# Optimization experiments

Hardware: AMD Instinct MI355X
Metric: run time of the kernel (lower is better)

Reference implementation:

```python
import jax, jax.numpy as jnp
import numpy as np

STRIDES = (8, 16, 32)
IMG = 640
REG_MAX = 16
TOPK = 10
ALPHA = 0.5
BETA = 6.0
EPS_IOU = 1e-16


def _make_anchors():
    # anchor centers for all pyramid levels, (N, 2) in pixel coords
    pts = []
    for s in STRIDES:
        h = w = IMG // s
        ys, xs = jnp.meshgrid(jnp.arange(h, dtype=jnp.float32),
                              jnp.arange(w, dtype=jnp.float32), indexing='ij')
        a = (jnp.stack([xs, ys], axis=-1).reshape(-1, 2) + 0.5) * s
        pts.append(a)
    return jnp.concatenate(pts, axis=0)  # (8400, 2)


def _iou_pairwise(pred, gt):
    # pred (B,N,4), gt (B,M,4) -> IoU (B,M,N)
    b1 = pred[:, None, :, :]   # (B,1,N,4)
    b2 = gt[:, :, None, :]     # (B,M,1,4)
    tl = jnp.maximum(b1[..., :2], b2[..., :2])
    br = jnp.minimum(b1[..., 2:], b2[..., 2:])
    wh = jnp.clip(br - tl, 0.0)
    inter = wh[..., 0] * wh[..., 1]
    a1 = (b1[..., 2] - b1[..., 0]) * (b1[..., 3] - b1[..., 1])
    a2 = (b2[..., 2] - b2[..., 0]) * (b2[..., 3] - b2[..., 1])
    return inter / (a1 + a2 - inter + EPS_IOU)


def _iou_1v1(b1, b2):
    # elementwise IoU, both (..., 4)
    tl = jnp.maximum(b1[..., :2], b2[..., :2])
    br = jnp.minimum(b1[..., 2:], b2[..., 2:])
    wh = jnp.clip(br - tl, 0.0)
    inter = wh[..., 0] * wh[..., 1]
    a1 = (b1[..., 2] - b1[..., 0]) * (b1[..., 3] - b1[..., 1])
    a2 = (b2[..., 2] - b2[..., 0]) * (b2[..., 3] - b2[..., 1])
    return inter / (a1 + a2 - inter + EPS_IOU)


def setup_inputs() -> dict:
    key = jax.random.key(0)
    ks = jax.random.split(key, 6)
    B, N, NC, M = 32, 8400, 80, 40
    pred_scores = jax.random.normal(ks[0], (B, N, NC), jnp.float32)
    pred_dist = jax.random.normal(ks[1], (B, N, 4 * REG_MAX), jnp.float32)
    gt_labels = jax.random.randint(ks[2], (B, M, 1), 0, NC, dtype=jnp.int32)
    cxy = jax.random.uniform(ks[3], (B, M, 2), jnp.float32) * 560.0 + 40.0
    wh = jax.random.uniform(ks[4], (B, M, 2), jnp.float32) * 120.0 + 20.0
    gt_bboxes = jnp.concatenate([jnp.clip(cxy - wh / 2, 0.0, float(IMG)),
                                 jnp.clip(cxy + wh / 2, 0.0, float(IMG))], axis=-1)
    dfl_weight = jax.random.normal(ks[5], (REG_MAX,), jnp.float32) * 0.05
    return {"pred_scores": pred_scores, "pred_dist": pred_dist,
            "gt_labels": gt_labels, "gt_bboxes": gt_bboxes,
            "dfl_weight": dfl_weight}


def reference(pred_scores, pred_dist, gt_labels, gt_bboxes, dfl_weight):
    B, N, NC = pred_scores.shape
    M = gt_bboxes.shape[1]
    anchors = _make_anchors()  # (N, 2)

    # DFL: softmax over reg bins, weighted sum with (random-init) conv weight
    prob = jax.nn.softmax(pred_dist.reshape(B, N, 4, REG_MAX), axis=-1)
    ltrb = prob @ dfl_weight                      # (B,N,4)
    pred_bboxes = jnp.concatenate([anchors - ltrb[..., :2],
                                   anchors + ltrb[..., 2:]], axis=-1)  # (B,N,4) xyxy

    # ---- task-aligned assigner (no-grad) ----
    sg = jax.lax.stop_gradient
    sig = jax.nn.sigmoid(sg(pred_scores))         # (B,N,NC)
    labels = gt_labels[..., 0].astype(jnp.int32)  # (B,M)
    sigT = jnp.swapaxes(sig, 1, 2)                # (B,NC,N)
    scores = jnp.take_along_axis(sigT, jnp.broadcast_to(labels[:, :, None], (B, M, N)), axis=1)  # (B,M,N)
    ious = jnp.clip(_iou_pairwise(sg(pred_bboxes), gt_bboxes), 0.0)      # (B,M,N)
    align = scores ** ALPHA * ious ** BETA        # (B,M,N)

    _, topk_idxs = jax.lax.top_k(align, TOPK)     # (B,M,TOPK) over anchors
    mask = jnp.zeros((B * M, N), dtype=align.dtype)
    mask = mask.at[jnp.arange(B * M)[:, None], topk_idxs.reshape(B * M, TOPK)].set(1.0)
    mask = mask.reshape(B, M, N)
    mask = mask * (align > 1e-9).astype(align.dtype)
    max_m = align.max(axis=1)                     # (B,N) best metric per anchor
    mask = mask * (align == max_m[:, None, :]).astype(align.dtype)

    fg_mask = mask.max(axis=1)                    # (B,N) in {0,1}
    tgt_idx = mask.argmax(axis=1)                 # (B,N) assigned gt index
    ts_sum = jnp.maximum(fg_mask.sum(), 1.0)

    # ---- classification targets (vectorized scatter) ----
    asg_labels = jnp.take_along_axis(labels, tgt_idx, axis=1)  # (B,N)
    target_scores = jax.nn.one_hot(asg_labels, NC, dtype=pred_scores.dtype) * (max_m * fg_mask)[..., None]

    x = pred_scores
    bce = jnp.maximum(x, 0.0) - x * target_scores + jnp.log1p(jnp.exp(-jnp.abs(x)))
    loss_cls = bce.sum() / ts_sum

    # ---- box IoU loss on positives (vectorized gather + mask) ----
    gt_asg = jnp.take_along_axis(gt_bboxes, tgt_idx[..., None], axis=1)  # (B,N,4)
    iou1 = _iou_1v1(pred_bboxes, gt_asg)          # (B,N)
    fg = fg_mask.sum()
    loss_box = jnp.where(fg > 0, ((1.0 - iou1) * fg_mask).sum() / fg, 0.0)

    return loss_cls + loss_box * 1.5
```

## Files before the change

kernel.cpp:

```cpp
#include <hip/hip_runtime.h>
#include <cstdint>
#include <cstddef>

#define BB 32
#define NN 8400
#define NCC 80
#define MM 40
#define RM 16
#define TOPKK 10
#define CAP 2048
#define SLOTP 41
#define AB 64

__device__ __forceinline__ void anchor_xy(int n, float& ax, float& ay) {
    int s, x, y;
    if (n < 6400)      { s = 8;  y = n / 80;            x = n - y * 80; }
    else if (n < 8000) { int i = n - 6400; s = 16; y = i / 40; x = i - y * 40; }
    else               { int i = n - 8000; s = 32; y = i / 20; x = i - y * 20; }
    ax = ((float)x + 0.5f) * (float)s;
    ay = ((float)y + 0.5f) * (float)s;
}

__global__ __launch_bounds__(256, 4) void k_mono(const float* __restrict__ ps,
                                                 const float* __restrict__ pd,
                                                 const int*   __restrict__ gl,
                                                 const float* __restrict__ gb,
                                                 const float* __restrict__ w,
                                                 float* __restrict__ pbb,
                                                 float* __restrict__ maxm,
                                                 int*   __restrict__ cnts,
                                                 unsigned long long* __restrict__ lists,
                                                 float* __restrict__ accum,
                                                 int*   __restrict__ tgt) {
    __shared__ float  sc[AB * SLOTP];
    __shared__ float  boxf[AB * 4];
    __shared__ float  gtb[MM * 4];
    __shared__ int    glab[MM];
    __shared__ int    slotm[MM];
    __shared__ int    cmap[NCC];
    __shared__ float  cm[256];
    __shared__ float  redf[4];
    const int b  = blockIdx.y;
    const int n0 = blockIdx.x * AB;
    const int t  = threadIdx.x;

    if (t < AB && n0 + t < NN) tgt[(size_t)b * NN + n0 + t] = 0x7F7F7F7F;

    const int a    = t >> 2, side = t & 3;
    const int nA   = n0 + a;
    const int ncA  = min(nA, NN - 1);
    const float* p = pd + (((size_t)(b * NN + ncA)) * 4 + side) * RM;
    float4 xa0 = *(const float4*)(p);
    float4 xa1 = *(const float4*)(p + 4);
    float4 xa2 = *(const float4*)(p + 8);
    float4 xa3 = *(const float4*)(p + 12);

    float4 vv[5];
    #pragma unroll
    for (int k = 0; k < 5; k++) {
        int f = t + k * 256;
        int row = f / 20, c4 = f - row * 20;
        int nc = min(n0 + row, NN - 1);
        vv[k] = *(const float4*)(ps + ((size_t)(b * NN + nc)) * NCC + c4 * 4);
    }

    if (t < MM * 4)              gtb[t] = gb[b * MM * 4 + t];
    if (t >= 192 && t < 192+MM)  glab[t - 192] = gl[b * MM + (t - 192)];
    if (t >= 96 && t < 96+NCC)   cmap[t - 96] = 0x7FFFFFFF;
    __syncthreads();
    if (t < MM) atomicMin(&cmap[glab[t]], t);
    __syncthreads();
    if (t < MM) slotm[t] = cmap[glab[t]];

    {
        float x[RM];
        x[0]=xa0.x;  x[1]=xa0.y;  x[2]=xa0.z;  x[3]=xa0.w;
        x[4]=xa1.x;  x[5]=xa1.y;  x[6]=xa1.z;  x[7]=xa1.w;
        x[8]=xa2.x;  x[9]=xa2.y;  x[10]=xa2.z; x[11]=xa2.w;
        x[12]=xa3.x; x[13]=xa3.y; x[14]=xa3.z; x[15]=xa3.w;
        float mx = x[0];
        #pragma unroll
        for (int i = 1; i < RM; i++) mx = fmaxf(mx, x[i]);
        float s = 0.f, d = 0.f;
        #pragma unroll
        for (int i = 0; i < RM; i++) {
            float e = __builtin_amdgcn_exp2f((x[i] - mx) * 1.44269504f);
            s += e; d += e * w[i];
        }
        d *= __builtin_amdgcn_rcpf(s);
        float ax, ay; anchor_xy(ncA, ax, ay);
        float axy = (side & 1) ? ay : ax;
        float v = (side < 2) ? (axy - d) : (axy + d);
        boxf[t] = v;
        if (nA < NN) pbb[((size_t)(b * NN + nA)) * 4 + side] = v;
    }

    float sp = 0.f;
    #pragma unroll
    for (int k = 0; k < 5; k++) {
        int f = t + k * 256;
        int row = f / 20, c4 = f - row * 20;
        float vmask = (n0 + row < NN) ? 1.f : 0.f;
        float xs[4] = {vv[k].x, vv[k].y, vv[k].z, vv[k].w};
        #pragma unroll
        for (int j = 0; j < 4; j++) {
            float x = xs[j];
            float e = __builtin_amdgcn_exp2f(-1.44269504f * fabsf(x));
            float r = __builtin_amdgcn_rcpf(1.0f + e);
            sp += vmask * (fmaxf(x, 0.f) + 0.69314718f * __builtin_amdgcn_logf(1.0f + e));
            int sl = cmap[c4 * 4 + j];
            if (sl < MM) sc[row * SLOTP + sl] = (x >= 0.f) ? r : e * r;
        }
    }
    __syncthreads();

    const int nloc = t & 63;
    const int n    = n0 + nloc;
    const int mb   = (t >> 6) * 10;
    const int lane = t & 63;
    const bool valid = (n < NN);
    float cmax = -INFINITY;
    float4 p4 = ((const float4*)boxf)[nloc];
    const float px1 = p4.x, py1 = p4.y, px2 = p4.z, py2 = p4.w;
    const float a1 = (px2 - px1) * (py2 - py1);
    #pragma unroll
    for (int j = 0; j < 10; j++) {
        int m = mb + j;
        float gx1 = gtb[m*4+0], gy1 = gtb[m*4+1], gx2 = gtb[m*4+2], gy2 = gtb[m*4+3];
        float a2 = (gx2 - gx1) * (gy2 - gy1);
        float iw = fmaxf(fminf(px2, gx2) - fmaxf(px1, gx1), 0.f);
        float ih = fmaxf(fminf(py2, gy2) - fmaxf(py1, gy1), 0.f);
        float inter = iw * ih;
        float iou = fmaxf(inter * __builtin_amdgcn_rcpf(a1 + a2 - inter + 1e-16f), 0.f);
        float al = 0.f;
        if (valid) {
            float sg = sc[nloc * SLOTP + slotm[m]];
            float i2 = iou * iou;
            al = __builtin_amdgcn_sqrtf(sg) * (i2 * i2 * i2);
        }
        cmax = fmaxf(cmax, al);
        bool pos = valid && (al > 1e-9f);
        unsigned long long msk = __ballot(pos);
        if (msk) {
            int leader = __ffsll((long long)msk) - 1;
            int basev = 0;
            if (lane == leader) basev = atomicAdd(&cnts[b * MM + m], __popcll(msk));
            basev = __shfl(basev, leader);
            if (pos) {
                int ofs = __popcll(msk & ((1ull << lane) - 1ull));
                int idx = basev + ofs;
                if (idx < CAP)
                    lists[((size_t)(b * MM + m)) * CAP + idx] =
                        ((unsigned long long)__float_as_uint(al) << 32) | (unsigned)n;
            }
        }
    }
    cm[t] = cmax;
    __syncthreads();
    if (t < AB && valid)
        maxm[(size_t)b * NN + n] =
            fmaxf(fmaxf(cm[t], cm[t + 64]), fmaxf(cm[t + 128], cm[t + 192]));

    #pragma unroll
    for (int off = 32; off > 0; off >>= 1) sp += __shfl_down(sp, off);
    if ((t & 63) == 0) redf[t >> 6] = sp;
    __syncthreads();
    if (t == 0) atomicAdd(accum, redf[0] + redf[1] + redf[2] + redf[3]);
}

__global__ __launch_bounds__(64) void k_topk(const unsigned long long* __restrict__ lists,
                                             const int*   __restrict__ cnts,
                                             const float* __restrict__ maxm,
                                             int* __restrict__ tgt) {
    __shared__ unsigned long long keys[CAP];
    __shared__ unsigned long long sel[TOPKK];
    const int bm = blockIdx.x, b = bm / MM, m = bm % MM, t = threadIdx.x;
    int cnt = min(cnts[bm], CAP);
    int kk = min(TOPKK, cnt);
    for (int i = t; i < cnt; i += 64) {
        unsigned long long L = lists[(size_t)bm * CAP + i];
        keys[i] = (L & 0xFFFFFFFF00000000ull) | (0xFFFFFFFFull - (L & 0xFFFFFFFFull));
    }
    __syncthreads();
    for (int p = 0; p < kk; p++) {
        unsigned long long best = 0ull;
        for (int i = t; i < cnt; i += 64) best = keys[i] > best ? keys[i] : best;
        #pragma unroll
        for (int off = 32; off > 0; off >>= 1) {
            unsigned long long o = __shfl_xor(best, off);
            best = o > best ? o : best;
        }
        for (int i = t; i < cnt; i += 64) if (keys[i] == best) keys[i] = 0ull;
        if (t == 0) sel[p] = best;
        __syncthreads();
    }
    if (t < kk) {
        unsigned long long bb = sel[t];
        float v = __uint_as_float((unsigned)(bb >> 32));
        int n = (int)(0xFFFFFFFFull - (bb & 0xFFFFFFFFull));
        if (v == maxm[(size_t)b * NN + n]) atomicMin(&tgt[(size_t)b * NN + n], m);
    }
}

__global__ __launch_bounds__(256) void k_fg(const int*   __restrict__ tgt,
                                            const int*   __restrict__ gl,
                                            const float* __restrict__ gb,
                                            const float* __restrict__ ps,
                                            const float* __restrict__ pbb,
                                            const float* __restrict__ maxm,
                                            float* __restrict__ accum) {
    int i = blockIdx.x * 256 + threadIdx.x;
    int t = threadIdx.x;
    float vdot = 0.f, vbox = 0.f, vfg = 0.f;
    int tg = tgt[i];
    if (tg < MM) {
        int b = i / NN;
        int lab = gl[b * MM + tg];
        float x = ps[(size_t)i * NCC + lab];
        float mm = maxm[i];
        float4 p = *(const float4*)(pbb + (size_t)i * 4);
        const float* g = gb + ((size_t)b * MM + tg) * 4;
        float a1 = (p.z - p.x) * (p.w - p.y);
        float a2 = (g[2] - g[0]) * (g[3] - g[1]);
        float iw = fmaxf(fminf(p.z, g[2]) - fmaxf(p.x, g[0]), 0.f);
        float ih = fmaxf(fminf(p.w, g[3]) - fmaxf(p.y, g[1]), 0.f);
        float inter = iw * ih;
        float iou = inter / (a1 + a2 - inter + 1e-16f);
        vdot = x * mm; vbox = 1.0f - iou; vfg = 1.0f;
    }
    #pragma unroll
    for (int off = 32; off > 0; off >>= 1) {
        vdot += __shfl_down(vdot, off);
        vbox += __shfl_down(vbox, off);
        vfg  += __shfl_down(vfg,  off);
    }
    __shared__ float r[3][4];
    if ((t & 63) == 0) { int wv = t >> 6; r[0][wv] = vdot; r[1][wv] = vbox; r[2][wv] = vfg; }
    __syncthreads();
    if (t < 3) {
        float s = r[t][0] + r[t][1] + r[t][2] + r[t][3];
        if (s != 0.f) atomicAdd(&accum[1 + t], s);
    }
}

__global__ void k_final(const float* __restrict__ accum, float* __restrict__ out) {
    float S0 = accum[0], dot = accum[1], box = accum[2], fg = accum[3];
    float ts = fmaxf(fg, 1.0f);
    float cls = (S0 - dot) / ts;
    float lb = (fg > 0.f) ? box / fg : 0.f;
    out[0] = cls + 1.5f * lb;
}

extern "C" void kernel_launch(void* const* d_in, const int* in_sizes, int n_in,
                              void* d_out, int out_size, void* d_ws, size_t ws_size,
                              hipStream_t stream) {
    const float* ps = (const float*)d_in[0];
    const float* pd = (const float*)d_in[1];
    const int*   gl = (const int*)  d_in[2];
    const float* gb = (const float*)d_in[3];
    const float* w  = (const float*)d_in[4];

    char* ws = (char*)d_ws;
    constexpr size_t ACC_BYTES  = 256;
    constexpr size_t CNT_BYTES  = 8192;
    constexpr size_t PBB_BYTES  = (size_t)BB * NN * 4 * sizeof(float);
    constexpr size_t MAXM_BYTES = (size_t)BB * NN * sizeof(float);
    constexpr size_t TGT_BYTES  = (size_t)BB * NN * sizeof(int);

    float* accum = (float*)ws;
    int*   cnts  = (int*)  (ws + ACC_BYTES);
    float* pbb   = (float*)(ws + ACC_BYTES + CNT_BYTES);
    float* maxm  = (float*)(ws + ACC_BYTES + CNT_BYTES + PBB_BYTES);
    int*   tgt   = (int*)  (ws + ACC_BYTES + CNT_BYTES + PBB_BYTES + MAXM_BYTES);
    unsigned long long* lists =
        (unsigned long long*)(ws + ACC_BYTES + CNT_BYTES + PBB_BYTES + MAXM_BYTES + TGT_BYTES);

    hipMemsetAsync(ws, 0, ACC_BYTES + CNT_BYTES, stream);

    dim3 gmono((NN + AB - 1) / AB, BB);
    k_mono<<<gmono, 256, 0, stream>>>(ps, pd, gl, gb, w, pbb, maxm, cnts, lists, accum, tgt);
    k_topk<<<BB * MM, 64, 0, stream>>>(lists, cnts, maxm, tgt);
    k_fg<<<BB * NN / 256, 256, 0, stream>>>(tgt, gl, gb, ps, pbb, maxm, accum);
    k_final<<<1, 1, 0, stream>>>(accum, (float*)d_out);
}
```

Before: 207.7 us.

## Make anchor work wave-local to drop block barriers in mono kernel

```diff
diff --git a/kernel.cpp b/kernel.cpp
--- a/kernel.cpp
+++ b/kernel.cpp
@@ -21,33 +21,44 @@
     ay = ((float)y + 0.5f) * (float)s;
 }
 
-__global__ __launch_bounds__(256, 4) void k_mono(const float* __restrict__ ps,
-                                                 const float* __restrict__ pd,
-                                                 const int*   __restrict__ gl,
-                                                 const float* __restrict__ gb,
-                                                 const float* __restrict__ w,
-                                                 float* __restrict__ pbb,
-                                                 float* __restrict__ maxm,
-                                                 int*   __restrict__ cnts,
-                                                 unsigned long long* __restrict__ lists,
-                                                 float* __restrict__ accum,
-                                                 int*   __restrict__ tgt) {
-    __shared__ float  sc[AB * SLOTP];
-    __shared__ float  boxf[AB * 4];
-    __shared__ float  gtb[MM * 4];
-    __shared__ int    glab[MM];
-    __shared__ int    slotm[MM];
-    __shared__ int    cmap[NCC];
-    __shared__ float  cm[256];
-    __shared__ float  redf[4];
+__global__ __launch_bounds__(256) void k_mono(const float* __restrict__ ps,
+                                              const float* __restrict__ pd,
+                                              const int*   __restrict__ gl,
+                                              const float* __restrict__ gb,
+                                              const float* __restrict__ w,
+                                              float* __restrict__ pbb,
+                                              float* __restrict__ maxm,
+                                              int*   __restrict__ cnts,
+                                              unsigned long long* __restrict__ lists,
+                                              float* __restrict__ accum,
+                                              int*   __restrict__ tgt) {
+    __shared__ float sc[4 * 16 * SLOTP];
+    __shared__ float boxf[AB * 4];
+    __shared__ float gtb[MM * 4];
+    __shared__ int   glab[MM];
+    __shared__ int   slotm[MM];
+    __shared__ int   cmap[NCC];
+    __shared__ float redf[4];
     const int b  = blockIdx.y;
     const int n0 = blockIdx.x * AB;
     const int t  = threadIdx.x;
+    const int wv = t >> 6;
+    const int l  = t & 63;
 
     if (t < AB && n0 + t < NN) tgt[(size_t)b * NN + n0 + t] = 0x7F7F7F7F;
 
-    const int a    = t >> 2, side = t & 3;
-    const int nA   = n0 + a;
+    if (t < MM * 4)              gtb[t] = gb[b * MM * 4 + t];
+    if (t >= 192 && t < 192+MM)  glab[t - 192] = gl[b * MM + (t - 192)];
+    if (t >= 96 && t < 96+NCC)   cmap[t - 96] = 0x7FFFFFFF;
+    __syncthreads();
+    if (t < MM) atomicMin(&cmap[glab[t]], t);
+    __syncthreads();
+    if (t < MM) slotm[t] = cmap[glab[t]];
+    __syncthreads();
+
+
+    const int aT   = t >> 2, side = t & 3;
+    const int nA   = n0 + aT;
     const int ncA  = min(nA, NN - 1);
     const float* p = pd + (((size_t)(b * NN + ncA)) * 4 + side) * RM;
     float4 xa0 = *(const float4*)(p);
@@ -58,19 +69,11 @@
     float4 vv[5];
     #pragma unroll
     for (int k = 0; k < 5; k++) {
-        int f = t + k * 256;
-        int row = f / 20, c4 = f - row * 20;
-        int nc = min(n0 + row, NN - 1);
+        int fl = l + k * 64;
+        int rl = fl / 20, c4 = fl - rl * 20;
+        int nc = min(n0 + wv * 16 + rl, NN - 1);
         vv[k] = *(const float4*)(ps + ((size_t)(b * NN + nc)) * NCC + c4 * 4);
     }
-
-    if (t < MM * 4)              gtb[t] = gb[b * MM * 4 + t];
-    if (t >= 192 && t < 192+MM)  glab[t - 192] = gl[b * MM + (t - 192)];
-    if (t >= 96 && t < 96+NCC)   cmap[t - 96] = 0x7FFFFFFF;
-    __syncthreads();
-    if (t < MM) atomicMin(&cmap[glab[t]], t);
-    __syncthreads();
-    if (t < MM) slotm[t] = cmap[glab[t]];
 
     {
         float x[RM];
@@ -98,9 +101,9 @@
     float sp = 0.f;
     #pragma unroll
     for (int k = 0; k < 5; k++) {
-        int f = t + k * 256;
-        int row = f / 20, c4 = f - row * 20;
-        float vmask = (n0 + row < NN) ? 1.f : 0.f;
+        int fl = l + k * 64;
+        int rl = fl / 20, c4 = fl - rl * 20;
+        float vmask = (n0 + wv * 16 + rl < NN) ? 1.f : 0.f;
         float xs[4] = {vv[k].x, vv[k].y, vv[k].z, vv[k].w};
         #pragma unroll
         for (int j = 0; j < 4; j++) {
@@ -109,23 +112,24 @@
             float r = __builtin_amdgcn_rcpf(1.0f + e);
             sp += vmask * (fmaxf(x, 0.f) + 0.69314718f * __builtin_amdgcn_logf(1.0f + e));
             int sl = cmap[c4 * 4 + j];
-            if (sl < MM) sc[row * SLOTP + sl] = (x >= 0.f) ? r : e * r;
-        }
-    }
-    __syncthreads();
-
-    const int nloc = t & 63;
-    const int n    = n0 + nloc;
-    const int mb   = (t >> 6) * 10;
-    const int lane = t & 63;
+            if (sl < MM) sc[(wv * 16 + rl) * SLOTP + sl] = (x >= 0.f) ? r : e * r;
+        }
+    }
+
+    asm volatile("s_waitcnt lgkmcnt(0)" ::: "memory");
+    __builtin_amdgcn_sched_barrier(0);
+
+    const int aL = l & 15;
+    const int g  = l >> 4;
+    const int n  = n0 + wv * 16 + aL;
     const bool valid = (n < NN);
     float cmax = -INFINITY;
-    float4 p4 = ((const float4*)boxf)[nloc];
+    float4 p4 = ((const float4*)boxf)[wv * 16 + aL];
     const float px1 = p4.x, py1 = p4.y, px2 = p4.z, py2 = p4.w;
     const float a1 = (px2 - px1) * (py2 - py1);
     #pragma unroll
     for (int j = 0; j < 10; j++) {
-        int m = mb + j;
+        int m = g * 10 + j;
         float gx1 = gtb[m*4+0], gy1 = gtb[m*4+1], gx2 = gtb[m*4+2], gy2 = gtb[m*4+3];
         float a2 = (gx2 - gx1) * (gy2 - gy1);
         float iw = fmaxf(fminf(px2, gx2) - fmaxf(px1, gx1), 0.f);
@@ -134,36 +138,26 @@
         float iou = fmaxf(inter * __builtin_amdgcn_rcpf(a1 + a2 - inter + 1e-16f), 0.f);
         float al = 0.f;
         if (valid) {
-            float sg = sc[nloc * SLOTP + slotm[m]];
+            float sg = sc[(wv * 16 + aL) * SLOTP + slotm[m]];
             float i2 = iou * iou;
             al = __builtin_amdgcn_sqrtf(sg) * (i2 * i2 * i2);
         }
         cmax = fmaxf(cmax, al);
-        bool pos = valid && (al > 1e-9f);
-        unsigned long long msk = __ballot(pos);
-        if (msk) {
-            int leader = __ffsll((long long)msk) - 1;
-            int basev = 0;
-            if (lane == leader) basev = atomicAdd(&cnts[b * MM + m], __popcll(msk));
-            basev = __shfl(basev, leader);
-            if (pos) {
-                int ofs = __popcll(msk & ((1ull << lane) - 1ull));
-                int idx = basev + ofs;
-                if (idx < CAP)
-                    lists[((size_t)(b * MM + m)) * CAP + idx] =
-                        ((unsigned long long)__float_as_uint(al) << 32) | (unsigned)n;
-            }
-        }
-    }
-    cm[t] = cmax;
-    __syncthreads();
-    if (t < AB && valid)
-        maxm[(size_t)b * NN + n] =
-            fmaxf(fmaxf(cm[t], cm[t + 64]), fmaxf(cm[t + 128], cm[t + 192]));
+        if (al > 1e-9f) {
+            int idx = atomicAdd(&cnts[b * MM + m], 1);
+            if (idx < CAP)
+                lists[((size_t)(b * MM + m)) * CAP + idx] =
+                    ((unsigned long long)__float_as_uint(al) << 32) | (unsigned)n;
+        }
+    }
+    cmax = fmaxf(cmax, __shfl_xor(cmax, 16));
+    cmax = fmaxf(cmax, __shfl_xor(cmax, 32));
+    if (l < 16 && valid) maxm[(size_t)b * NN + n] = cmax;
+
 
     #pragma unroll
     for (int off = 32; off > 0; off >>= 1) sp += __shfl_down(sp, off);
-    if ((t & 63) == 0) redf[t >> 6] = sp;
+    if (l == 0) redf[wv] = sp;
     __syncthreads();
     if (t == 0) atomicAdd(accum, redf[0] + redf[1] + redf[2] + redf[3]);
 }
```

New measurement: 205.0 us. Within noise of the previous version (-1.3%).
